# Kernel optimization log

Hardware: AMD Instinct MI355X
Metric: run time of the kernel (lower is better)

Reference implementation:

```python
import jax, jax.numpy as jnp
import numpy as np
from jax import lax

# QKeras quantized_bits(8, 0, alpha=1, keep_negative=1):
#   delta = 2^-(bits-1) = 1/128, q(x) = clip(round(x*128), -128, 127)/128
QB_SCALE = 128.0
# QKeras quantized_relu(8, 0): q(x) = clip(round(x*256), 0, 255)/256
QR_SCALE = 256.0

def _ste(q, x):
    # straight-through estimator: forward = q(x), backward = identity
    return x + lax.stop_gradient(q - x)

def qbits(x):
    q = jnp.clip(jnp.round(x * QB_SCALE), -QB_SCALE, QB_SCALE - 1.0) / QB_SCALE
    return _ste(q, x)

def qrelu(x):
    q = jnp.clip(jnp.round(x * QR_SCALE), 0.0, QR_SCALE - 1.0) / QR_SCALE
    return _ste(q, x)


def setup_inputs() -> dict:
    key = jax.random.key(0)
    ks = jax.random.split(key, 9)
    B, C, F = 1000000, 16, 3
    dims = [C * F, 64, 32, 32]
    x = jax.random.normal(ks[0], (B, C, F), dtype=jnp.float32)
    def w(k, i, o):
        return jax.random.normal(k, (i, o), dtype=jnp.float32) * (0.5 / np.sqrt(i))
    inp = {"x": x}
    for li in range(3):
        inp[f"w{li+1}"] = w(ks[1 + 2 * li], dims[li], dims[li + 1])
        inp[f"b{li+1}"] = jax.random.normal(ks[2 + 2 * li], (dims[li + 1],), dtype=jnp.float32) * 0.05
    inp["wout"] = w(ks[7], dims[-1], 5)
    inp["bout"] = jax.random.normal(ks[8], (5,), dtype=jnp.float32) * 0.05
    return inp


def reference(x, w1, b1, w2, b2, w3, b3, wout, bout):
    h = x.reshape(x.shape[0], -1)  # Flatten: [B, 48]
    for w, b in ((w1, b1), (w2, b2), (w3, b3)):
        # QDense: fake-quantize kernel & bias, fp32 matmul, quantized_relu
        h = qrelu(h @ qbits(w) + qbits(b))
    return h @ wout + bout  # final float Dense -> logits [B, 5]
```

## Files before the change

### kernel.cpp

```cpp
#include <hip/hip_runtime.h>
#include <hip/hip_bf16.h>

typedef short  short8 __attribute__((ext_vector_type(8)));
typedef float  f32x4  __attribute__((ext_vector_type(4)));
typedef unsigned int u32;
typedef unsigned long long u64;
typedef unsigned short u16;

__device__ __forceinline__ u32 f2bf(float v) {
    u32 u = __float_as_uint(v);
    return (u + 0x7FFFu + ((u >> 16) & 1u)) >> 16;
}
__device__ __forceinline__ float qround128(float w) {
    float q = rintf(w * 128.0f);
    return fminf(fmaxf(q, -128.0f), 127.0f);
}
__device__ __forceinline__ u32 cvtpk(float a, float b) {
    __hip_bfloat162 h = __float22bfloat162_rn(make_float2(a, b));
    union { __hip_bfloat162 h; u32 u; } cv; cv.h = h; return cv.u;
}
__device__ __forceinline__ float q255(float v) {
    return fminf(fmaxf(rintf(v), 0.f), 255.f);
}
union FragU { short8 s; u32 u[4]; };
__device__ __forceinline__ short8 pack2(f32x4 a, f32x4 b) {
    FragU f;
    f.u[0] = cvtpk(q255(a[0]), q255(a[1]));
    f.u[1] = cvtpk(q255(a[2]), q255(a[3]));
    f.u[2] = cvtpk(q255(b[0]), q255(b[1]));
    f.u[3] = cvtpk(q255(b[2]), q255(b[3]));
    return f.s;
}
__device__ __forceinline__ f32x4 mfma16(short8 a, short8 b, f32x4 c) {
    return __builtin_amdgcn_mfma_f32_16x16x32_bf16(a, b, c, 0, 0, 0);
}


__global__ void prep(const float* __restrict__ w1, const float* __restrict__ b1,
                     const float* __restrict__ w2, const float* __restrict__ b2,
                     const float* __restrict__ w3, const float* __restrict__ b3,
                     const float* __restrict__ wo, const float* __restrict__ bo,
                     u16* __restrict__ wsh) {
    int t = threadIdx.x;
    for (int idx = t; idx < 16 * 512; idx += 256) {
        int blk = idx >> 9, e = idx & 511;
        int l = e >> 3, j = e & 7;
        int r  = l & 15;
        int gi = l >> 4;
        int kk = gi * 8 + j;
        int fp = 16 * (j >> 2) + 4 * gi + (j & 3);
        float val = 0.f;
        if (blk < 8) {
            int mt = blk >> 1, ks = blk & 1;
            int k = ks * 32 + kk, fo = mt * 16 + r;
            if (k < 48) val = 2.0f * qround128(w1[k * 64 + fo]);
        } else if (blk < 12) {
            int bi = blk - 8, mt = bi >> 1, ks = bi & 1;
            int f = ks * 32 + fp, fo = mt * 16 + r;
            val = qround128(w2[f * 32 + fo]) * (1.0f / 128.0f);
        } else if (blk < 14) {
            int mt = blk - 12;
            val = qround128(w3[fp * 32 + mt * 16 + r]) * (1.0f / 128.0f);
        } else {
            float wv = (r < 5) ? wo[fp * 5 + r] * (1.0f / 256.0f) : 0.f;
            u32 hb = f2bf(wv);
            if (blk == 14) { wsh[idx] = (u16)hb; continue; }
            val = wv - __uint_as_float(hb << 16);
        }
        wsh[idx] = (u16)f2bf(val);
    }
    float* wsf = (float*)(wsh + 8192);
    for (int i = t; i < 64; i += 256) wsf[i]       = 2.0f * qround128(b1[i]);
    for (int i = t; i < 32; i += 256) wsf[64 + i]  = 2.0f * qround128(b2[i]);
    for (int i = t; i < 32; i += 256) wsf[96 + i]  = 2.0f * qround128(b3[i]);
    for (int i = t; i < 16; i += 256) wsf[128 + i] = (i < 5) ? bo[i] : 0.f;
}


__global__ __launch_bounds__(256, 2) void mlp_mfma(const float* __restrict__ x,
                                                   const u16* __restrict__ wsh,
                                                   float* __restrict__ out, int ntiles) {
    const int tid = threadIdx.x;
    const int wid = tid >> 6, lane = tid & 63;
    const int c = lane & 15, g = lane >> 4;

    short8 wf[16];
    const short8* wv = (const short8*)wsh;
    #pragma unroll
    for (int i = 0; i < 16; ++i) wf[i] = wv[i * 64 + lane];

    const float* wsf = (const float*)(wsh + 8192);
    f32x4 b1q[4], b2q[2], b3q[2], boq;
    #pragma unroll
    for (int i = 0; i < 4; ++i) b1q[i] = *(const f32x4*)(wsf + i * 16 + 4 * g);
    #pragma unroll
    for (int i = 0; i < 2; ++i) b2q[i] = *(const f32x4*)(wsf + 64 + i * 16 + 4 * g);
    #pragma unroll
    for (int i = 0; i < 2; ++i) b3q[i] = *(const f32x4*)(wsf + 96 + i * 16 + 4 * g);
    boq = *(const f32x4*)(wsf + 128 + 4 * g);

    const int xoff = c * 48 + g * 8;
    const int gw = blockIdx.x * 4 + wid;
    const int nw = gridDim.x * 4;
    const f32x4 zero4 = {0.f, 0.f, 0.f, 0.f};

    for (int t0 = gw; t0 < ntiles; t0 += nw) {
        const float* xl = x + (size_t)t0 * 768 + xoff;
        float4 xa = *(const float4*)(xl);
        float4 xb = *(const float4*)(xl + 4);
        float4 xc = make_float4(0.f, 0.f, 0.f, 0.f);
        float4 xd = make_float4(0.f, 0.f, 0.f, 0.f);
        if (g < 2) { xc = *(const float4*)(xl + 32); xd = *(const float4*)(xl + 36); }

        float v0[8] = {xa.x, xa.y, xa.z, xa.w, xb.x, xb.y, xb.z, xb.w};
        float v1[8] = {xc.x, xc.y, xc.z, xc.w, xd.x, xd.y, xd.z, xd.w};
        FragU bh0, bl0, bh1, bl1;
        #pragma unroll
        for (int p = 0; p < 4; ++p) {
            u32 uu = cvtpk(v0[2 * p], v0[2 * p + 1]);
            bh0.u[p] = uu;
            float r0 = v0[2 * p]     - __uint_as_float(uu << 16);
            float r1 = v0[2 * p + 1] - __uint_as_float(uu & 0xFFFF0000u);
            bl0.u[p] = cvtpk(r0, r1);
            u32 ww = cvtpk(v1[2 * p], v1[2 * p + 1]);
            bh1.u[p] = ww;
            float s0 = v1[2 * p]     - __uint_as_float(ww << 16);
            float s1 = v1[2 * p + 1] - __uint_as_float(ww & 0xFFFF0000u);
            bl1.u[p] = cvtpk(s0, s1);
        }

        f32x4 acc1[4];
        #pragma unroll
        for (int mt = 0; mt < 4; ++mt) {
            f32x4 ah = mfma16(wf[mt * 2 + 0], bh0.s, b1q[mt]);
            ah = mfma16(wf[mt * 2 + 1], bh1.s, ah);
            f32x4 al = mfma16(wf[mt * 2 + 0], bl0.s, zero4);
            al = mfma16(wf[mt * 2 + 1], bl1.s, al);
            acc1[mt] = ah + al;
        }

        short8 p0 = pack2(acc1[0], acc1[1]);
        short8 p1 = pack2(acc1[2], acc1[3]);

        f32x4 a20 = mfma16(wf[8],  p0, b2q[0]);
        f32x4 a21 = mfma16(wf[9],  p1, zero4);
        f32x4 a22 = mfma16(wf[10], p0, b2q[1]);
        f32x4 a23 = mfma16(wf[11], p1, zero4);
        short8 p2 = pack2(a20 + a21, a22 + a23);

        f32x4 a30 = mfma16(wf[12], p2, b3q[0]);
        f32x4 a31 = mfma16(wf[13], p2, b3q[1]);
        short8 p3 = pack2(a30, a31);

        f32x4 aoh = mfma16(wf[14], p3, boq);
        f32x4 aol = mfma16(wf[15], p3, zero4);
        f32x4 ao = aoh + aol;

        float* orow = out + (size_t)t0 * 80 + c * 5;
        if (g == 0) {
            orow[0] = ao[0]; orow[1] = ao[1]; orow[2] = ao[2]; orow[3] = ao[3];
        } else if (g == 1) {
            orow[4] = ao[0];
        }
    }
}

extern "C" void kernel_launch(void* const* d_in, const int* in_sizes, int n_in,
                              void* d_out, int out_size, void* d_ws, size_t ws_size,
                              hipStream_t stream) {
    const float* x  = (const float*)d_in[0];
    const float* w1 = (const float*)d_in[1];
    const float* b1 = (const float*)d_in[2];
    const float* w2 = (const float*)d_in[3];
    const float* b2 = (const float*)d_in[4];
    const float* w3 = (const float*)d_in[5];
    const float* b3 = (const float*)d_in[6];
    const float* wo = (const float*)d_in[7];
    const float* bo = (const float*)d_in[8];
    float* out = (float*)d_out;

    int B = in_sizes[0] / 48;
    int ntiles = B / 16;

    prep<<<1, 256, 0, stream>>>(w1, b1, w2, b2, w3, b3, wo, bo, (u16*)d_ws);

    int blocks = (ntiles + 3) / 4;
    if (blocks > 2048) blocks = 2048;
    mlp_mfma<<<blocks, 256, 0, stream>>>(x, (const u16*)d_ws, out, ntiles);
}
```

Before: 59.10 us.

## Batch four tiles per wave, uniform 12-float x loads, fold bias into layer-1 MFMA

Each wave now handles a pack of four 16-row tiles. It issues all x loads for the pack up front, and every lane reads a uniform 12-float slice instead of a divergent 8/16 split. The layer-1 K layout is remapped so each lane group covers 12 contiguous inputs. The b1 bias is folded in as an extra weight row multiplied by a constant-1 input slot, which removes the bias registers. The prep kernel is spread over 32 blocks, one element per thread, instead of a single block looping. The goal is more memory-level parallelism and fewer wasted loads, at the cost of more registers and a smaller grid.

New measurement: 51.74 us. 1.14x faster.

```diff
diff --git a/kernel.cpp b/kernel.cpp
--- a/kernel.cpp
+++ b/kernel.cpp
@@ -41,19 +41,24 @@
                      const float* __restrict__ w3, const float* __restrict__ b3,
                      const float* __restrict__ wo, const float* __restrict__ bo,
                      u16* __restrict__ wsh) {
-    int t = threadIdx.x;
-    for (int idx = t; idx < 16 * 512; idx += 256) {
+    int idx = blockIdx.x * 256 + threadIdx.x;
+    if (idx < 16 * 512) {
         int blk = idx >> 9, e = idx & 511;
         int l = e >> 3, j = e & 7;
         int r  = l & 15;
         int gi = l >> 4;
-        int kk = gi * 8 + j;
         int fp = 16 * (j >> 2) + 4 * gi + (j & 3);
         float val = 0.f;
         if (blk < 8) {
             int mt = blk >> 1, ks = blk & 1;
-            int k = ks * 32 + kk, fo = mt * 16 + r;
-            if (k < 48) val = 2.0f * qround128(w1[k * 64 + fo]);
+            int fo = mt * 16 + r;
+            if (ks == 0) {
+                val = 2.0f * qround128(w1[(12 * gi + j) * 64 + fo]);
+            } else if (j < 4) {
+                val = 2.0f * qround128(w1[(12 * gi + 8 + j) * 64 + fo]);
+            } else if (gi == 3 && j == 7) {
+                val = 2.0f * qround128(b1[fo]);
+            }
         } else if (blk < 12) {
             int bi = blk - 8, mt = bi >> 1, ks = bi & 1;
             int f = ks * 32 + fp, fo = mt * 16 + r;
@@ -64,16 +69,18 @@
         } else {
             float wv = (r < 5) ? wo[fp * 5 + r] * (1.0f / 256.0f) : 0.f;
             u32 hb = f2bf(wv);
-            if (blk == 14) { wsh[idx] = (u16)hb; continue; }
+            if (blk == 14) { wsh[idx] = (u16)hb; return; }
             val = wv - __uint_as_float(hb << 16);
         }
         wsh[idx] = (u16)f2bf(val);
     }
-    float* wsf = (float*)(wsh + 8192);
-    for (int i = t; i < 64; i += 256) wsf[i]       = 2.0f * qround128(b1[i]);
-    for (int i = t; i < 32; i += 256) wsf[64 + i]  = 2.0f * qround128(b2[i]);
-    for (int i = t; i < 32; i += 256) wsf[96 + i]  = 2.0f * qround128(b3[i]);
-    for (int i = t; i < 16; i += 256) wsf[128 + i] = (i < 5) ? bo[i] : 0.f;
+    if (blockIdx.x == 0) {
+        int t = threadIdx.x;
+        float* wsf = (float*)(wsh + 8192);
+        for (int i = t; i < 32; i += 256) wsf[64 + i]  = 2.0f * qround128(b2[i]);
+        for (int i = t; i < 32; i += 256) wsf[96 + i]  = 2.0f * qround128(b3[i]);
+        for (int i = t; i < 16; i += 256) wsf[128 + i] = (i < 5) ? bo[i] : 0.f;
+    }
 }
 
 
@@ -90,77 +97,92 @@
     for (int i = 0; i < 16; ++i) wf[i] = wv[i * 64 + lane];
 
     const float* wsf = (const float*)(wsh + 8192);
-    f32x4 b1q[4], b2q[2], b3q[2], boq;
-    #pragma unroll
-    for (int i = 0; i < 4; ++i) b1q[i] = *(const f32x4*)(wsf + i * 16 + 4 * g);
+    f32x4 b2q[2], b3q[2], boq;
     #pragma unroll
     for (int i = 0; i < 2; ++i) b2q[i] = *(const f32x4*)(wsf + 64 + i * 16 + 4 * g);
     #pragma unroll
     for (int i = 0; i < 2; ++i) b3q[i] = *(const f32x4*)(wsf + 96 + i * 16 + 4 * g);
     boq = *(const f32x4*)(wsf + 128 + 4 * g);
 
-    const int xoff = c * 48 + g * 8;
+    const int xoff = c * 48 + g * 12;
+    const int npacks = (ntiles + 3) >> 2;
     const int gw = blockIdx.x * 4 + wid;
     const int nw = gridDim.x * 4;
     const f32x4 zero4 = {0.f, 0.f, 0.f, 0.f};
 
-    for (int t0 = gw; t0 < ntiles; t0 += nw) {
-        const float* xl = x + (size_t)t0 * 768 + xoff;
-        float4 xa = *(const float4*)(xl);
-        float4 xb = *(const float4*)(xl + 4);
-        float4 xc = make_float4(0.f, 0.f, 0.f, 0.f);
-        float4 xd = make_float4(0.f, 0.f, 0.f, 0.f);
-        if (g < 2) { xc = *(const float4*)(xl + 32); xd = *(const float4*)(xl + 36); }
-
-        float v0[8] = {xa.x, xa.y, xa.z, xa.w, xb.x, xb.y, xb.z, xb.w};
-        float v1[8] = {xc.x, xc.y, xc.z, xc.w, xd.x, xd.y, xd.z, xd.w};
-        FragU bh0, bl0, bh1, bl1;
+    for (int p = gw; p < npacks; p += nw) {
+        float4 xq0[4], xq1[4], xq2[4];
         #pragma unroll
-        for (int p = 0; p < 4; ++p) {
-            u32 uu = cvtpk(v0[2 * p], v0[2 * p + 1]);
-            bh0.u[p] = uu;
-            float r0 = v0[2 * p]     - __uint_as_float(uu << 16);
-            float r1 = v0[2 * p + 1] - __uint_as_float(uu & 0xFFFF0000u);
-            bl0.u[p] = cvtpk(r0, r1);
-            u32 ww = cvtpk(v1[2 * p], v1[2 * p + 1]);
-            bh1.u[p] = ww;
-            float s0 = v1[2 * p]     - __uint_as_float(ww << 16);
-            float s1 = v1[2 * p + 1] - __uint_as_float(ww & 0xFFFF0000u);
-            bl1.u[p] = cvtpk(s0, s1);
+        for (int i = 0; i < 4; ++i) {
+            int t = 4 * p + i;
+            int tl = (t < ntiles) ? t : (ntiles - 1);
+            const float* xl = x + (size_t)tl * 768 + xoff;
+            xq0[i] = *(const float4*)(xl);
+            xq1[i] = *(const float4*)(xl + 4);
+            xq2[i] = *(const float4*)(xl + 8);
         }
 
-        f32x4 acc1[4];
         #pragma unroll
-        for (int mt = 0; mt < 4; ++mt) {
-            f32x4 ah = mfma16(wf[mt * 2 + 0], bh0.s, b1q[mt]);
-            ah = mfma16(wf[mt * 2 + 1], bh1.s, ah);
-            f32x4 al = mfma16(wf[mt * 2 + 0], bl0.s, zero4);
-            al = mfma16(wf[mt * 2 + 1], bl1.s, al);
-            acc1[mt] = ah + al;
-        }
-
-        short8 p0 = pack2(acc1[0], acc1[1]);
-        short8 p1 = pack2(acc1[2], acc1[3]);
-
-        f32x4 a20 = mfma16(wf[8],  p0, b2q[0]);
-        f32x4 a21 = mfma16(wf[9],  p1, zero4);
-        f32x4 a22 = mfma16(wf[10], p0, b2q[1]);
-        f32x4 a23 = mfma16(wf[11], p1, zero4);
-        short8 p2 = pack2(a20 + a21, a22 + a23);
-
-        f32x4 a30 = mfma16(wf[12], p2, b3q[0]);
-        f32x4 a31 = mfma16(wf[13], p2, b3q[1]);
-        short8 p3 = pack2(a30, a31);
-
-        f32x4 aoh = mfma16(wf[14], p3, boq);
-        f32x4 aol = mfma16(wf[15], p3, zero4);
-        f32x4 ao = aoh + aol;
-
-        float* orow = out + (size_t)t0 * 80 + c * 5;
-        if (g == 0) {
-            orow[0] = ao[0]; orow[1] = ao[1]; orow[2] = ao[2]; orow[3] = ao[3];
-        } else if (g == 1) {
-            orow[4] = ao[0];
+        for (int i = 0; i < 4; ++i) {
+            float v[12] = {xq0[i].x, xq0[i].y, xq0[i].z, xq0[i].w,
+                           xq1[i].x, xq1[i].y, xq1[i].z, xq1[i].w,
+                           xq2[i].x, xq2[i].y, xq2[i].z, xq2[i].w};
+            FragU bh0, bl0, bh1, bl1;
+            #pragma unroll
+            for (int q = 0; q < 4; ++q) {
+                u32 uu = cvtpk(v[2 * q], v[2 * q + 1]);
+                bh0.u[q] = uu;
+                float r0 = v[2 * q]     - __uint_as_float(uu << 16);
+                float r1 = v[2 * q + 1] - __uint_as_float(uu & 0xFFFF0000u);
+                bl0.u[q] = cvtpk(r0, r1);
+            }
+            #pragma unroll
+            for (int q = 0; q < 2; ++q) {
+                u32 uu = cvtpk(v[8 + 2 * q], v[9 + 2 * q]);
+                bh1.u[q] = uu;
+                float r0 = v[8 + 2 * q] - __uint_as_float(uu << 16);
+                float r1 = v[9 + 2 * q] - __uint_as_float(uu & 0xFFFF0000u);
+                bl1.u[q] = cvtpk(r0, r1);
+            }
+            bh1.u[2] = 0u;
+            bh1.u[3] = (g == 3) ? 0x3F800000u : 0u;
+            bl1.u[2] = 0u; bl1.u[3] = 0u;
+
+            f32x4 acc1[4];
+            #pragma unroll
+            for (int mt = 0; mt < 4; ++mt) {
+                f32x4 ah = mfma16(wf[mt * 2 + 0], bh0.s, zero4);
+                ah = mfma16(wf[mt * 2 + 1], bh1.s, ah);
+                f32x4 al = mfma16(wf[mt * 2 + 0], bl0.s, zero4);
+                al = mfma16(wf[mt * 2 + 1], bl1.s, al);
+                acc1[mt] = ah + al;
+            }
+            short8 p0 = pack2(acc1[0], acc1[1]);
+            short8 p1 = pack2(acc1[2], acc1[3]);
+
+            f32x4 a20 = mfma16(wf[8],  p0, b2q[0]);
+            f32x4 a21 = mfma16(wf[9],  p1, zero4);
+            f32x4 a22 = mfma16(wf[10], p0, b2q[1]);
+            f32x4 a23 = mfma16(wf[11], p1, zero4);
+            short8 p2 = pack2(a20 + a21, a22 + a23);
+
+            f32x4 a30 = mfma16(wf[12], p2, b3q[0]);
+            f32x4 a31 = mfma16(wf[13], p2, b3q[1]);
+            short8 p3 = pack2(a30, a31);
+
+            f32x4 aoh = mfma16(wf[14], p3, boq);
+            f32x4 aol = mfma16(wf[15], p3, zero4);
+            f32x4 ao = aoh + aol;
+
+            int t = 4 * p + i;
+            if (t < ntiles) {
+                float* orow = out + (size_t)t * 80 + c * 5;
+                if (g == 0) {
+                    orow[0] = ao[0]; orow[1] = ao[1]; orow[2] = ao[2]; orow[3] = ao[3];
+                } else if (g == 1) {
+                    orow[4] = ao[0];
+                }
+            }
         }
     }
 }
@@ -181,10 +203,11 @@
 
     int B = in_sizes[0] / 48;
     int ntiles = B / 16;
-
-    prep<<<1, 256, 0, stream>>>(w1, b1, w2, b2, w3, b3, wo, bo, (u16*)d_ws);
-
-    int blocks = (ntiles + 3) / 4;
+    int npacks = (ntiles + 3) / 4;
+
+    prep<<<32, 256, 0, stream>>>(w1, b1, w2, b2, w3, b3, wo, bo, (u16*)d_ws);
+
+    int blocks = (npacks + 7) / 8;
     if (blocks > 2048) blocks = 2048;
     mlp_mfma<<<blocks, 256, 0, stream>>>(x, (const u16*)d_ws, out, ntiles);
 }
```
